# Kernel optimization log

Measured on AMD Instinct MI355X. Metric: run time of the kernel, lower is better.

## Reference

```python
import jax, jax.numpy as jnp
import numpy as np

B, IN, N, K = 8192, 1024, 4096, 409
BN_EPS = 1e-5
BOOST_STRENGTH = 1.0


def setup_inputs() -> dict:
    key = jax.random.key(0)
    k1, k2, k3, k4, k5 = jax.random.split(key, 5)
    x = jax.random.normal(k1, (B, IN), dtype=jnp.float32)
    W = jax.random.normal(k2, (N, IN), dtype=jnp.float32) * 0.03
    b = jax.random.normal(k3, (N,), dtype=jnp.float32) * 0.01
    wmask = jax.random.randint(k4, (N, IN), 0, 2, dtype=jnp.int32)
    dutyCycle = jax.random.uniform(k5, (N,), dtype=jnp.float32) * (K / N) * 2.0
    return {"x": x, "W": W, "b": b, "wmask": wmask, "dutyCycle": dutyCycle, "k": K}


def reference(x, W, b, wmask, dutyCycle, k):
    n = W.shape[0]
    # rezeroWeights: enforce fixed weight sparsity pattern
    Wm = W * wmask.astype(W.dtype)
    # Linear
    y = jnp.einsum("bi,ni->bn", x, Wm) + b
    # BatchNorm1d(affine=False), training mode: batch mean / biased variance
    mean = jnp.mean(y, axis=0)
    var = jnp.mean(jnp.square(y - mean), axis=0)
    y = (y - mean) / jnp.sqrt(var + BN_EPS)
    # KWinners with duty-cycle boosting (k < n path)
    targetDensity = jnp.float32(k) / n
    boostFactors = jnp.exp((targetDensity - dutyCycle) * BOOST_STRENGTH)
    boosted = jax.lax.stop_gradient(y) * boostFactors  # [B, n]
    _, idx = jax.lax.top_k(boosted, k)                 # [B, k]
    rows = jnp.arange(y.shape[0])[:, None]
    out = jnp.zeros_like(y).at[rows, idx].set(jnp.take_along_axis(y, idx, axis=1))
    return out
```

## Files before the change

### kernel.cpp

```cpp
#include <hip/hip_runtime.h>

#define BATCH 8192
#define INF   1024
#define NF    4096
#define BN_EPS 1e-5
#define NT    32

typedef __attribute__((ext_vector_type(8))) short short8v;
typedef __attribute__((ext_vector_type(4))) float f32x4;

#define FENCE asm volatile("" ::: "memory")
#define BARRIER do { FENCE; __builtin_amdgcn_s_barrier(); FENCE; } while (0)

__global__ void zero_ws(double* __restrict__ p) {
    p[blockIdx.x * 256 + threadIdx.x] = 0.0;
}

__device__ __forceinline__ void split3(float x, ushort& h0, ushort& h1, ushort& h2) {
    const unsigned u0 = __float_as_uint(x) & 0xFFFF0000u;
    const float    r1 = x - __uint_as_float(u0);
    const unsigned u1 = __float_as_uint(r1) & 0xFFFF0000u;
    const float    r2 = r1 - __uint_as_float(u1);
    h0 = (ushort)(u0 >> 16);
    h1 = (ushort)(u1 >> 16);
    h2 = (ushort)(__float_as_uint(r2) >> 16);
}

__global__ __launch_bounds__(256) void split_x_kernel(
    const float* __restrict__ X, ushort* __restrict__ xs)
{
    const size_t base = ((size_t)blockIdx.x * 256 + threadIdx.x) * 8;
    const size_t LS = (size_t)BATCH * INF;
    const float4 v0 = *(const float4*)(X + base);
    const float4 v1 = *(const float4*)(X + base + 4);
    const float v[8] = {v0.x, v0.y, v0.z, v0.w, v1.x, v1.y, v1.z, v1.w};
    short8v s0, s1, s2;
#pragma unroll
    for (int i = 0; i < 8; ++i) {
        ushort h0, h1, h2;
        split3(v[i], h0, h1, h2);
        s0[i] = (short)h0; s1[i] = (short)h1; s2[i] = (short)h2;
    }
    *(short8v*)&xs[base]          = s0;
    *(short8v*)&xs[base + LS]     = s1;
    *(short8v*)&xs[base + 2 * LS] = s2;
}

__global__ __launch_bounds__(256) void split_w_kernel(
    const float* __restrict__ W, const int* __restrict__ Mk, ushort* __restrict__ wsp)
{
    const size_t base = ((size_t)blockIdx.x * 256 + threadIdx.x) * 8;
    const size_t LS = (size_t)NF * INF;
    const float4 v0 = *(const float4*)(W + base);
    const float4 v1 = *(const float4*)(W + base + 4);
    const int4   m0 = *(const int4*)(Mk + base);
    const int4   m1 = *(const int4*)(Mk + base + 4);
    const float v[8] = {v0.x * (float)m0.x, v0.y * (float)m0.y,
                        v0.z * (float)m0.z, v0.w * (float)m0.w,
                        v1.x * (float)m1.x, v1.y * (float)m1.y,
                        v1.z * (float)m1.z, v1.w * (float)m1.w};
    short8v s0, s1, s2;
#pragma unroll
    for (int i = 0; i < 8; ++i) {
        ushort h0, h1, h2;
        split3(v[i], h0, h1, h2);
        s0[i] = (short)h0; s1[i] = (short)h1; s2[i] = (short)h2;
    }
    *(short8v*)&wsp[base]          = s0;
    *(short8v*)&wsp[base + LS]     = s1;
    *(short8v*)&wsp[base + 2 * LS] = s2;
}

__device__ __forceinline__ void gload16(const ushort* g, ushort* l) {
    __builtin_amdgcn_global_load_lds(
        (const __attribute__((address_space(1))) void*)g,
        (__attribute__((address_space(3))) void*)l, 16, 0, 0);
}

__global__ __launch_bounds__(512) void gemm_mfma_fuse(
    const ushort* __restrict__ Xs, const ushort* __restrict__ Wsp,
    const float* __restrict__ bias, float* __restrict__ Y,
    double* __restrict__ dsum, double* __restrict__ dsqs)
{
    extern __shared__ ushort sm[];
    const size_t LSX = (size_t)BATCH * INF;
    const size_t LSW = (size_t)NF * INF;

    const int t    = threadIdx.x;
    const int row0 = blockIdx.y * 128;
    const int col0 = blockIdx.x * 128;

    const int l   = t & 63;
    const int l15 = l & 15;
    const int hi  = l >> 4;
    const int wid = t >> 6;
    const int wm  = wid >> 1;
    const int wn  = wid & 1;

    const int srow  = t >> 2;
    const int sunit = (t & 3) ^ ((t >> 3) & 3);
    const int uoff = (hi ^ ((l15 >> 1) & 3)) << 3;

    f32x4  acc[2][4];
    double mst[2][4][4];
#pragma unroll
    for (int mf = 0; mf < 2; ++mf)
#pragma unroll
        for (int nf = 0; nf < 4; ++nf) {
            acc[mf][nf] = (f32x4){0.f, 0.f, 0.f, 0.f};
#pragma unroll
            for (int r = 0; r < 4; ++r) mst[mf][nf][r] = 0.0;
        }

#define PB(b, p) (sm + (b) * 24576 + (p) * 4096)

#pragma unroll
    for (int tt = 0; tt < 2; ++tt) {
#pragma unroll
        for (int p = 0; p < 3; ++p)
            gload16(Xs + (size_t)p * LSX + (size_t)(row0 + srow) * INF + tt * 32 + sunit * 8,
                    PB(tt, p) + (size_t)t * 8);
#pragma unroll
        for (int p = 0; p < 3; ++p)
            gload16(Wsp + (size_t)p * LSW + (size_t)(col0 + srow) * INF + tt * 32 + sunit * 8,
                    PB(tt, 3 + p) + (size_t)t * 8);
    }
    asm volatile("s_waitcnt vmcnt(6)" ::: "memory");
    BARRIER;

#define TILE(tt, CUR, DST) do {                                               \
    if ((tt) + 2 < NT) {                                                      \
        const int kof_ = ((tt) + 2) * 32;                                     \
        _Pragma("unroll")                                                     \
        for (int p = 0; p < 3; ++p)                                           \
            gload16(Xs + (size_t)p * LSX + (size_t)(row0 + srow) * INF + kof_ + sunit * 8, \
                    PB(DST, p) + (size_t)t * 8);                              \
        _Pragma("unroll")                                                     \
        for (int p = 0; p < 3; ++p)                                           \
            gload16(Wsp + (size_t)p * LSW + (size_t)(col0 + srow) * INF + kof_ + sunit * 8, \
                    PB(DST, 3 + p) + (size_t)t * 8);                          \
    }                                                                         \
    short8v A_[2][3], B_[4][3];                                               \
    _Pragma("unroll")                                                         \
    for (int mf = 0; mf < 2; ++mf) {                                          \
        const int ra = (wm * 32 + mf * 16 + l15) * 32 + uoff;                 \
        _Pragma("unroll")                                                     \
        for (int p = 0; p < 3; ++p)                                           \
            A_[mf][p] = *(const short8v*)&PB(CUR, p)[ra];                     \
    }                                                                         \
    _Pragma("unroll")                                                         \
    for (int nf = 0; nf < 4; ++nf) {                                          \
        const int rb = (wn * 64 + nf * 16 + l15) * 32 + uoff;                 \
        _Pragma("unroll")                                                     \
        for (int p = 0; p < 3; ++p)                                           \
            B_[nf][p] = *(const short8v*)&PB(CUR, 3 + p)[rb];                 \
    }                                                                         \
    __builtin_amdgcn_s_setprio(1);                                            \
    _Pragma("unroll")                                                         \
    for (int mf = 0; mf < 2; ++mf)                                            \
        _Pragma("unroll")                                                     \
        for (int nf = 0; nf < 4; ++nf) {                                      \
            f32x4 c = acc[mf][nf];                                            \
            c = __builtin_amdgcn_mfma_f32_16x16x32_bf16(A_[mf][0], B_[nf][0], c, 0, 0, 0); \
            c = __builtin_amdgcn_mfma_f32_16x16x32_bf16(A_[mf][0], B_[nf][1], c, 0, 0, 0); \
            c = __builtin_amdgcn_mfma_f32_16x16x32_bf16(A_[mf][1], B_[nf][0], c, 0, 0, 0); \
            c = __builtin_amdgcn_mfma_f32_16x16x32_bf16(A_[mf][0], B_[nf][2], c, 0, 0, 0); \
            c = __builtin_amdgcn_mfma_f32_16x16x32_bf16(A_[mf][1], B_[nf][1], c, 0, 0, 0); \
            c = __builtin_amdgcn_mfma_f32_16x16x32_bf16(A_[mf][2], B_[nf][0], c, 0, 0, 0); \
            acc[mf][nf] = c;                                                  \
        }                                                                     \
    __builtin_amdgcn_s_setprio(0);                                            \
    if ((tt) & 1) {                                                           \
        _Pragma("unroll")                                                     \
        for (int mf = 0; mf < 2; ++mf)                                        \
            _Pragma("unroll")                                                 \
            for (int nf = 0; nf < 4; ++nf) {                                  \
                _Pragma("unroll")                                             \
                for (int r = 0; r < 4; ++r)                                   \
                    mst[mf][nf][r] += (double)acc[mf][nf][r];                 \
                acc[mf][nf] = (f32x4){0.f, 0.f, 0.f, 0.f};                    \
            }                                                                 \
    }                                                                         \
    if ((tt) < NT - 2)       { asm volatile("s_waitcnt vmcnt(6)" ::: "memory"); } \
    else if ((tt) == NT - 2) { asm volatile("s_waitcnt vmcnt(0)" ::: "memory"); } \
    BARRIER;                                                                  \
} while (0)

    for (int tb = 0; tb + 3 <= NT; tb += 3) {
        TILE(tb,     0, 2);
        TILE(tb + 1, 1, 0);
        TILE(tb + 2, 2, 1);
    }
    TILE(30, 0, 2);
    TILE(31, 1, 0);
#undef TILE
#undef PB

    double* sdsum = (double*)sm;
    double* sdsqs = sdsum + 16 * 128;
    const int grp = wm * 4 + hi;
#pragma unroll
    for (int nf = 0; nf < 4; ++nf) {
        const int colL = wn * 64 + nf * 16 + l15;
        const int colc = col0 + colL;
        const double bb = (double)bias[colc];
        double s = 0.0, q = 0.0;
#pragma unroll
        for (int mf = 0; mf < 2; ++mf)
#pragma unroll
            for (int r = 0; r < 4; ++r) {
                const int roww = row0 + wm * 32 + mf * 16 + hi * 4 + r;
                const float yval = (float)(mst[mf][nf][r] + bb);
                Y[(size_t)roww * NF + colc] = yval;
                s += (double)yval;
                q += (double)yval * (double)yval;
            }
        sdsum[grp * 128 + colL] = s;
        sdsqs[grp * 128 + colL] = q;
    }
    __syncthreads();
    if (t < 128) {
        double s = 0.0;
#pragma unroll
        for (int g = 0; g < 16; ++g) s += sdsum[g * 128 + t];
        atomicAdd(&dsum[col0 + t], s);
    } else if (t < 256) {
        const int c = t - 128;
        double q = 0.0;
#pragma unroll
        for (int g = 0; g < 16; ++g) q += sdsqs[g * 128 + c];
        atomicAdd(&dsqs[col0 + c], q);
    }
}

__global__ __launch_bounds__(512) void gemm_mfma_split(
    const float* __restrict__ X, const float* __restrict__ W,
    const int* __restrict__ Mk, const float* __restrict__ bias,
    float* __restrict__ Y)
{
    __shared__ __align__(16) ushort a0s[128 * 40];
    __shared__ __align__(16) ushort a1s[128 * 40];
    __shared__ __align__(16) ushort a2s[128 * 40];
    __shared__ __align__(16) ushort b0s[128 * 40];
    __shared__ __align__(16) ushort b1s[128 * 40];
    __shared__ __align__(16) ushort b2s[128 * 40];

    const int t = threadIdx.x;
    const int row0 = blockIdx.y * 128;
    const int col0 = blockIdx.x * 128;
    const int srow = t >> 2;
    const int skb  = (t & 3) * 8;

    const float* Xp = X + (size_t)(row0 + srow) * INF + skb;
    const float* Wp = W + (size_t)(col0 + srow) * INF + skb;
    const int*   Mp = Mk + (size_t)(col0 + srow) * INF + skb;

    const int l   = t & 63;
    const int l15 = l & 15;
    const int hi  = l >> 4;
    const int wid = t >> 6;
    const int wm  = wid >> 1;
    const int wn  = wid & 1;

    f32x4  acc[2][4];
    double sh[2][4][4];
#pragma unroll
    for (int mf = 0; mf < 2; ++mf)
#pragma unroll
        for (int nf = 0; nf < 4; ++nf) {
            acc[mf][nf] = (f32x4){0.f, 0.f, 0.f, 0.f};
#pragma unroll
            for (int r = 0; r < 4; ++r) sh[mf][nf][r] = 0.0;
        }

    float4 xA0 = *(const float4*)(Xp);
    float4 xA1 = *(const float4*)(Xp + 4);
    float4 wB0 = *(const float4*)(Wp);
    float4 wB1 = *(const float4*)(Wp + 4);
    int4   mB0 = *(const int4*)(Mp);
    int4   mB1 = *(const int4*)(Mp + 4);

    for (int k0 = 0; k0 < INF; k0 += 32) {
        __syncthreads();
        {
            const float v[8] = {xA0.x, xA0.y, xA0.z, xA0.w, xA1.x, xA1.y, xA1.z, xA1.w};
            short8v s0, s1, s2;
#pragma unroll
            for (int i = 0; i < 8; ++i) {
                ushort h0, h1, h2;
                split3(v[i], h0, h1, h2);
                s0[i] = (short)h0; s1[i] = (short)h1; s2[i] = (short)h2;
            }
            const int off = srow * 40 + skb;
            *(short8v*)&a0s[off] = s0;
            *(short8v*)&a1s[off] = s1;
            *(short8v*)&a2s[off] = s2;
        }
        {
            const float wv[8] = {wB0.x * (float)mB0.x, wB0.y * (float)mB0.y,
                                 wB0.z * (float)mB0.z, wB0.w * (float)mB0.w,
                                 wB1.x * (float)mB1.x, wB1.y * (float)mB1.y,
                                 wB1.z * (float)mB1.z, wB1.w * (float)mB1.w};
            short8v s0, s1, s2;
#pragma unroll
            for (int i = 0; i < 8; ++i) {
                ushort h0, h1, h2;
                split3(wv[i], h0, h1, h2);
                s0[i] = (short)h0; s1[i] = (short)h1; s2[i] = (short)h2;
            }
            const int off = srow * 40 + skb;
            *(short8v*)&b0s[off] = s0;
            *(short8v*)&b1s[off] = s1;
            *(short8v*)&b2s[off] = s2;
        }
        __syncthreads();

        if (k0 + 32 < INF) {
            const int kn = k0 + 32;
            xA0 = *(const float4*)(Xp + kn);
            xA1 = *(const float4*)(Xp + kn + 4);
            wB0 = *(const float4*)(Wp + kn);
            wB1 = *(const float4*)(Wp + kn + 4);
            mB0 = *(const int4*)(Mp + kn);
            mB1 = *(const int4*)(Mp + kn + 4);
        }

        short8v A[2][3], B[4][3];
#pragma unroll
        for (int mf = 0; mf < 2; ++mf) {
            const int roff = (wm * 32 + mf * 16 + l15) * 40 + hi * 8;
            A[mf][0] = *(const short8v*)&a0s[roff];
            A[mf][1] = *(const short8v*)&a1s[roff];
            A[mf][2] = *(const short8v*)&a2s[roff];
        }
#pragma unroll
        for (int nf = 0; nf < 4; ++nf) {
            const int roff = (wn * 64 + nf * 16 + l15) * 40 + hi * 8;
            B[nf][0] = *(const short8v*)&b0s[roff];
            B[nf][1] = *(const short8v*)&b1s[roff];
            B[nf][2] = *(const short8v*)&b2s[roff];
        }

#pragma unroll
        for (int mf = 0; mf < 2; ++mf)
#pragma unroll
            for (int nf = 0; nf < 4; ++nf) {
                f32x4 c = acc[mf][nf];
                c = __builtin_amdgcn_mfma_f32_16x16x32_bf16(A[mf][0], B[nf][0], c, 0, 0, 0);
                c = __builtin_amdgcn_mfma_f32_16x16x32_bf16(A[mf][0], B[nf][1], c, 0, 0, 0);
                c = __builtin_amdgcn_mfma_f32_16x16x32_bf16(A[mf][1], B[nf][0], c, 0, 0, 0);
                c = __builtin_amdgcn_mfma_f32_16x16x32_bf16(A[mf][0], B[nf][2], c, 0, 0, 0);
                c = __builtin_amdgcn_mfma_f32_16x16x32_bf16(A[mf][1], B[nf][1], c, 0, 0, 0);
                c = __builtin_amdgcn_mfma_f32_16x16x32_bf16(A[mf][2], B[nf][0], c, 0, 0, 0);
                acc[mf][nf] = c;
            }

        if (k0 & 32) {
#pragma unroll
            for (int mf = 0; mf < 2; ++mf)
#pragma unroll
                for (int nf = 0; nf < 4; ++nf) {
#pragma unroll
                    for (int r = 0; r < 4; ++r) sh[mf][nf][r] += (double)acc[mf][nf][r];
                    acc[mf][nf] = (f32x4){0.f, 0.f, 0.f, 0.f};
                }
        }
    }

#pragma unroll
    for (int mf = 0; mf < 2; ++mf)
#pragma unroll
        for (int nf = 0; nf < 4; ++nf) {
            const int col = col0 + wn * 64 + nf * 16 + l15;
            const double bb = (double)bias[col];
#pragma unroll
            for (int r = 0; r < 4; ++r) {
                const int row = row0 + wm * 32 + mf * 16 + hi * 4 + r;
                Y[(size_t)row * NF + col] = (float)(sh[mf][nf][r] + bb);
            }
        }
}

__global__ __launch_bounds__(256) void stats_partial(
    const float* __restrict__ Y, double* __restrict__ dsum, double* __restrict__ dsqs)
{
    const int col = blockIdx.x * 256 + threadIdx.x;
    const int r0  = blockIdx.y * 256;
    double s = 0.0, ss = 0.0;
    for (int i = 0; i < 256; ++i) {
        const float v = Y[(size_t)(r0 + i) * NF + col];
        s  += (double)v;
        ss += (double)v * (double)v;
    }
    atomicAdd(&dsum[col], s);
    atomicAdd(&dsqs[col], ss);
}

__global__ __launch_bounds__(256) void stats_final(
    const double* __restrict__ dsum, const double* __restrict__ dsqs,
    const float* __restrict__ duty, const int* __restrict__ kp,
    double* __restrict__ mean64, double* __restrict__ rstd64, double* __restrict__ boost64,
    float* __restrict__ mean32, float* __restrict__ rstd32, float* __restrict__ boost32)
{
    const int c = blockIdx.x * 256 + threadIdx.x;
    const double m   = dsum[c] / (double)BATCH;
    const double var = dsqs[c] / (double)BATCH - m * m;
    const double rs  = 1.0 / sqrt(var + (double)BN_EPS);
    const double td  = (double)(*kp) / (double)NF;
    const double bf  = exp(td - (double)duty[c]);
    mean64[c] = m;  rstd64[c] = rs;  boost64[c] = bf;
    mean32[c] = (float)m; rstd32[c] = (float)rs; boost32[c] = (float)bf;
}

#define BAND 1e-4f
#define MAXCAND 64
#define LCAP 512

__global__ __launch_bounds__(256) void topk_kernel(
    const float* __restrict__ mean32, const float* __restrict__ rstd32,
    const float* __restrict__ boost32,
    const double* __restrict__ mean64, const double* __restrict__ rstd64,
    const double* __restrict__ boost64,
    const int* __restrict__ kp,
    const float* __restrict__ X, const float* __restrict__ W,
    const int* __restrict__ Mk, const float* __restrict__ bias,
    float* __restrict__ Y)
{
    __shared__ float    yv[NF];
    __shared__ unsigned keys[NF];
    __shared__ unsigned hist[256];
    __shared__ unsigned scan[256];
    __shared__ unsigned wtot[4];
    __shared__ unsigned s_bin, s_below;
    __shared__ int      s_cnt;
    __shared__ unsigned lkey[LCAP];
    __shared__ double   red[256];
    __shared__ int      s_ncand, s_H;
    __shared__ int      cand_idx[MAXCAND];
    __shared__ double   cand_val[MAXCAND];
    __shared__ unsigned char cand_pick[MAXCAND];

    const int r = blockIdx.x;
    const int t = threadIdx.x;
    const int K = *kp;
    const int lane = t & 63;
    const int w    = t >> 6;

    for (int j = 0; j < 4; ++j) {
        const int n = j * 1024 + t * 4;
        const float4 v  = *(const float4*)&Y[(size_t)r * NF + n];
        const float4 mm = *(const float4*)&mean32[n];
        const float4 rs = *(const float4*)&rstd32[n];
        const float4 bo = *(const float4*)&boost32[n];
        const float yb[4] = {(v.x - mm.x) * rs.x, (v.y - mm.y) * rs.y,
                             (v.z - mm.z) * rs.z, (v.w - mm.w) * rs.w};
        const float bsv[4] = {yb[0] * bo.x, yb[1] * bo.y, yb[2] * bo.z, yb[3] * bo.w};
#pragma unroll
        for (int q = 0; q < 4; ++q) {
            yv[n + q] = yb[q];
            unsigned u = __float_as_uint(bsv[q]);
            u ^= (u & 0x80000000u) ? 0xFFFFFFFFu : 0x80000000u;
            keys[n + q] = u;
        }
    }
    __syncthreads();

#define SUFFIX_SCAN() do {                                                    \
    unsigned v_ = hist[t];                                                    \
    _Pragma("unroll")                                                         \
    for (int off_ = 1; off_ < 64; off_ <<= 1) {                               \
        const unsigned o_ = __shfl_down(v_, off_, 64);                        \
        if (lane + off_ < 64) v_ += o_;                                       \
    }                                                                         \
    if (lane == 0) wtot[w] = v_;                                              \
    __syncthreads();                                                          \
    unsigned add_ = 0;                                                        \
    for (int ww_ = w + 1; ww_ < 4; ++ww_) add_ += wtot[ww_];                  \
    scan[t] = v_ + add_;                                                      \
    __syncthreads();                                                          \
} while (0)

    hist[t] = 0u;
    __syncthreads();
    for (int j = 0; j < 16; ++j)
        atomicAdd(&hist[keys[j * 256 + t] >> 24], 1u);
    __syncthreads();
    SUFFIX_SCAN();
    int remaining = K;
    if (scan[t] >= (unsigned)remaining &&
        (t == 255 || scan[t + 1] < (unsigned)remaining)) {
        s_bin = (unsigned)t;
        s_below = (t == 255) ? 0u : scan[t + 1];
    }
    if (t == 0) s_cnt = 0;
    __syncthreads();
    const unsigned b1 = s_bin;
    unsigned curval = b1 << 24;
    unsigned curmask = 0xFF000000u;
    remaining -= (int)s_below;
    __syncthreads();

    for (int j = 0; j < 16; ++j) {
        const unsigned u = keys[j * 256 + t];
        if ((u >> 24) == b1) {
            const int slot = atomicAdd(&s_cnt, 1);
            if (slot < LCAP) lkey[slot] = u;
        }
    }
    __syncthreads();
    const bool smallbin = (s_cnt <= LCAP);
    const int cnt = s_cnt;

    for (int pass = 2; pass >= 0; --pass) {
        const int sh = pass * 8;
        hist[t] = 0u;
        __syncthreads();
        if (smallbin) {
            for (int i = t; i < cnt; i += 256) {
                const unsigned u = lkey[i];
                if ((u & curmask) == curval)
                    atomicAdd(&hist[(u >> sh) & 255u], 1u);
            }
        } else {
            for (int j = 0; j < 16; ++j) {
                const unsigned u = keys[j * 256 + t];
                if ((u & curmask) == curval)
                    atomicAdd(&hist[(u >> sh) & 255u], 1u);
            }
        }
        __syncthreads();
        SUFFIX_SCAN();
        if (scan[t] >= (unsigned)remaining &&
            (t == 255 || scan[t + 1] < (unsigned)remaining)) {
            s_bin = (unsigned)t;
            s_below = (t == 255) ? 0u : scan[t + 1];
        }
        __syncthreads();
        curval |= (s_bin << sh);
        curmask |= (255u << sh);
        remaining -= (int)s_below;
        __syncthreads();
    }
#undef SUFFIX_SCAN

    const unsigned T = curval;
    const unsigned vT = (T & 0x80000000u) ? (T ^ 0x80000000u) : ~T;
    const float cut32 = __uint_as_float(vT);
    const float cutHi = cut32 + BAND;
    const float cutLo = cut32 - BAND;

    if (t == 0) { s_ncand = 0; s_H = 0; }
    __syncthreads();
    int locH = 0;
    for (int j = 0; j < 16; ++j) {
        const int n = j * 256 + t;
        const float b = yv[n] * boost32[n];
        if (b > cutHi) {
            locH++;
        } else if (b >= cutLo) {
            const int slot = atomicAdd(&s_ncand, 1);
            if (slot < MAXCAND) cand_idx[slot] = n;
        }
    }
    atomicAdd(&s_H, locH);
    __syncthreads();
    const int H = s_H;
    const bool overflow = (s_ncand > MAXCAND);
    const int ncand = overflow ? MAXCAND : s_ncand;
    int need = K - H;
    if (need < 0) need = 0;

    if (!overflow) {
        for (int c = 0; c < ncand; ++c) {
            const int n = cand_idx[c];
            const float* xr = X + (size_t)r * INF;
            const float* wn = W + (size_t)n * INF;
            const int*   mn = Mk + (size_t)n * INF;
            double s = 0.0;
            for (int i = t; i < INF; i += 256)
                s += (double)xr[i] * (double)(wn[i] * (float)mn[i]);
            red[t] = s;
            __syncthreads();
            for (int off = 128; off > 0; off >>= 1) {
                if (t < off) red[t] += red[t + off];
                __syncthreads();
            }
            if (t == 0) {
                const double y64 = red[0] + (double)bias[n];
                cand_val[c] = (y64 - mean64[n]) * rstd64[n] * boost64[n];
                cand_pick[c] = 0;
            }
            __syncthreads();
        }
        if (t == 0) {
            for (int p = 0; p < need; ++p) {
                int best = -1;
                for (int c = 0; c < ncand; ++c) {
                    if (cand_pick[c]) continue;
                    if (best < 0 || cand_val[c] > cand_val[best] ||
                        (cand_val[c] == cand_val[best] && cand_idx[c] < cand_idx[best]))
                        best = c;
                }
                if (best < 0) break;
                cand_pick[best] = 1;
            }
        }
        __syncthreads();
        for (int j = 0; j < 16; ++j) {
            const int n = j * 256 + t;
            const float b = yv[n] * boost32[n];
            keys[n] = (b > cutHi) ? 1u : 0u;
        }
        __syncthreads();
        if (t < ncand && cand_pick[t]) keys[cand_idx[t]] = 1u;
        __syncthreads();
    } else {
        const int fneed = remaining;
        unsigned cntk = 0u;
        for (int j = 0; j < 16; ++j) cntk += (keys[t * 16 + j] == T) ? 1u : 0u;
        scan[t] = cntk;
        __syncthreads();
        for (int off = 1; off < 256; off <<= 1) {
            const unsigned add = (t >= off) ? scan[t - off] : 0u;
            __syncthreads();
            scan[t] += add;
            __syncthreads();
        }
        unsigned rank = scan[t] - cntk;
        for (int j = 0; j < 16; ++j) {
            const int n = t * 16 + j;
            const unsigned u = keys[n];
            bool sel;
            if (u == T) { sel = ((int)rank < fneed); rank++; }
            else        { sel = (u > T); }
            keys[n] = sel ? 1u : 0u;
        }
        __syncthreads();
    }

    for (int j = 0; j < 4; ++j) {
        const int n = j * 1024 + t * 4;
        float4 o;
        o.x = keys[n + 0] ? yv[n + 0] : 0.0f;
        o.y = keys[n + 1] ? yv[n + 1] : 0.0f;
        o.z = keys[n + 2] ? yv[n + 2] : 0.0f;
        o.w = keys[n + 3] ? yv[n + 3] : 0.0f;
        *(float4*)&Y[(size_t)r * NF + n] = o;
    }
}

extern "C" void kernel_launch(void* const* d_in, const int* in_sizes, int n_in,
                              void* d_out, int out_size, void* d_ws, size_t ws_size,
                              hipStream_t stream)
{
    const float* x     = (const float*)d_in[0];
    const float* W     = (const float*)d_in[1];
    const float* b     = (const float*)d_in[2];
    const int*   wmask = (const int*)d_in[3];
    const float* duty  = (const float*)d_in[4];
    const int*   kp    = (const int*)d_in[5];
    float* out = (float*)d_out;

    const size_t SPLIT_X_ELTS = (size_t)3 * BATCH * INF;
    const size_t SPLIT_W_ELTS = (size_t)3 * NF * INF;
    const size_t STATS_BYTES  = (size_t)5 * NF * sizeof(double) + (size_t)3 * NF * sizeof(float);
    const size_t NEED_FAST    = (SPLIT_X_ELTS + SPLIT_W_ELTS) * sizeof(ushort) + STATS_BYTES;
    const bool fast = (ws_size >= NEED_FAST);

    ushort* xs  = (ushort*)d_ws;
    ushort* wsp = xs + SPLIT_X_ELTS;
    char* statbase = fast ? (char*)(wsp + SPLIT_W_ELTS) : (char*)d_ws;

    double* dsum    = (double*)statbase;
    double* dsqs    = dsum + NF;
    double* mean64  = dsqs + NF;
    double* rstd64  = mean64 + NF;
    double* boost64 = rstd64 + NF;
    float*  mean32  = (float*)(boost64 + NF);
    float*  rstd32  = mean32 + NF;
    float*  boost32 = rstd32 + NF;

    hipLaunchKernelGGL(zero_ws, dim3(2 * NF / 256), dim3(256), 0, stream, dsum);

    if (fast) {
        hipLaunchKernelGGL(split_x_kernel, dim3(BATCH * INF / 8 / 256), dim3(256), 0, stream,
                           x, xs);
        hipLaunchKernelGGL(split_w_kernel, dim3(NF * INF / 8 / 256), dim3(256), 0, stream,
                           W, wmask, wsp);
        hipFuncSetAttribute((const void*)gemm_mfma_fuse,
                            hipFuncAttributeMaxDynamicSharedMemorySize, 147456);
        hipLaunchKernelGGL(gemm_mfma_fuse, dim3(NF / 128, BATCH / 128), dim3(512), 147456,
                           stream, xs, wsp, b, out, dsum, dsqs);
    } else {
        hipLaunchKernelGGL(gemm_mfma_split, dim3(NF / 128, BATCH / 128), dim3(512), 0, stream,
                           x, W, wmask, b, out);
        hipLaunchKernelGGL(stats_partial, dim3(NF / 256, BATCH / 256), dim3(256), 0, stream,
                           out, dsum, dsqs);
    }

    hipLaunchKernelGGL(stats_final, dim3(NF / 256), dim3(256), 0, stream,
                       dsum, dsqs, duty, kp,
                       mean64, rstd64, boost64, mean32, rstd32, boost32);
    hipLaunchKernelGGL(topk_kernel, dim3(BATCH), dim3(256), 0, stream,
                       mean32, rstd32, boost32, mean64, rstd64, boost64, kp,
                       x, W, wmask, b, out);
}
```

Baseline: 558.3 us.

## Merge prep kernels and stats zeroing, streamline top-k key marking

Folds the stats-buffer zeroing and the separate x and W split kernels into one prep launch, so the fast path saves two kernel launches. In the top-k kernel, the selection flags are written during the candidate scan, which removes a later pass that recomputed the boosted values. The tie-breaking path now recomputes the order-preserving keys from yv and boost because the keys array has been overwritten. LCAP is raised to 768 so larger bins can use the compact candidate list, at the cost of more shared memory.

```diff
diff --git a/kernel.cpp b/kernel.cpp
--- a/kernel.cpp
+++ b/kernel.cpp
@@ -11,10 +11,6 @@
 
 #define FENCE asm volatile("" ::: "memory")
 #define BARRIER do { FENCE; __builtin_amdgcn_s_barrier(); FENCE; } while (0)
-
-__global__ void zero_ws(double* __restrict__ p) {
-    p[blockIdx.x * 256 + threadIdx.x] = 0.0;
-}
 
 __device__ __forceinline__ void split3(float x, ushort& h0, ushort& h1, ushort& h2) {
     const unsigned u0 = __float_as_uint(x) & 0xFFFF0000u;
@@ -26,49 +22,60 @@
     h2 = (ushort)(__float_as_uint(r2) >> 16);
 }
 
-__global__ __launch_bounds__(256) void split_x_kernel(
-    const float* __restrict__ X, ushort* __restrict__ xs)
+__global__ __launch_bounds__(256) void prep_kernel(
+    const float* __restrict__ X, const float* __restrict__ W,
+    const int* __restrict__ Mk,
+    ushort* __restrict__ xs, ushort* __restrict__ wsp,
+    double* __restrict__ dz)
 {
-    const size_t base = ((size_t)blockIdx.x * 256 + threadIdx.x) * 8;
-    const size_t LS = (size_t)BATCH * INF;
-    const float4 v0 = *(const float4*)(X + base);
-    const float4 v1 = *(const float4*)(X + base + 4);
-    const float v[8] = {v0.x, v0.y, v0.z, v0.w, v1.x, v1.y, v1.z, v1.w};
-    short8v s0, s1, s2;
-#pragma unroll
-    for (int i = 0; i < 8; ++i) {
-        ushort h0, h1, h2;
-        split3(v[i], h0, h1, h2);
-        s0[i] = (short)h0; s1[i] = (short)h1; s2[i] = (short)h2;
-    }
-    *(short8v*)&xs[base]          = s0;
-    *(short8v*)&xs[base + LS]     = s1;
-    *(short8v*)&xs[base + 2 * LS] = s2;
-}
-
-__global__ __launch_bounds__(256) void split_w_kernel(
-    const float* __restrict__ W, const int* __restrict__ Mk, ushort* __restrict__ wsp)
-{
-    const size_t base = ((size_t)blockIdx.x * 256 + threadIdx.x) * 8;
-    const size_t LS = (size_t)NF * INF;
-    const float4 v0 = *(const float4*)(W + base);
-    const float4 v1 = *(const float4*)(W + base + 4);
-    const int4   m0 = *(const int4*)(Mk + base);
-    const int4   m1 = *(const int4*)(Mk + base + 4);
-    const float v[8] = {v0.x * (float)m0.x, v0.y * (float)m0.y,
-                        v0.z * (float)m0.z, v0.w * (float)m0.w,
-                        v1.x * (float)m1.x, v1.y * (float)m1.y,
-                        v1.z * (float)m1.z, v1.w * (float)m1.w};
-    short8v s0, s1, s2;
-#pragma unroll
-    for (int i = 0; i < 8; ++i) {
-        ushort h0, h1, h2;
-        split3(v[i], h0, h1, h2);
-        s0[i] = (short)h0; s1[i] = (short)h1; s2[i] = (short)h2;
-    }
-    *(short8v*)&wsp[base]          = s0;
-    *(short8v*)&wsp[base + LS]     = s1;
-    *(short8v*)&wsp[base + 2 * LS] = s2;
+    const int blk = blockIdx.x;
+    const int t   = threadIdx.x;
+    if (blk == 0) {
+#pragma unroll
+        for (int i = 0; i < 32; ++i) dz[i * 256 + t] = 0.0;
+    }
+    if (blk < 4096) {
+        const size_t base = ((size_t)blk * 256 + t) * 8;
+        const size_t LS = (size_t)BATCH * INF;
+        const float4 v0 = *(const float4*)(X + base);
+        const float4 v1 = *(const float4*)(X + base + 4);
+        const float v[8] = {v0.x, v0.y, v0.z, v0.w, v1.x, v1.y, v1.z, v1.w};
+        short8v s0, s1, s2;
+#pragma unroll
+        for (int i = 0; i < 8; ++i) {
+            ushort h0, h1, h2;
+            split3(v[i], h0, h1, h2);
+            s0[i] = (short)h0; s1[i] = (short)h1; s2[i] = (short)h2;
+        }
+        *(short8v*)&xs[base]          = s0;
+        *(short8v*)&xs[base + LS]     = s1;
+        *(short8v*)&xs[base + 2 * LS] = s2;
+    } else {
+        const size_t base = ((size_t)(blk - 4096) * 256 + t) * 8;
+        const size_t LS = (size_t)NF * INF;
+        const float4 v0 = *(const float4*)(W + base);
+        const float4 v1 = *(const float4*)(W + base + 4);
+        const int4   m0 = *(const int4*)(Mk + base);
+        const int4   m1 = *(const int4*)(Mk + base + 4);
+        const float v[8] = {v0.x * (float)m0.x, v0.y * (float)m0.y,
+                            v0.z * (float)m0.z, v0.w * (float)m0.w,
+                            v1.x * (float)m1.x, v1.y * (float)m1.y,
+                            v1.z * (float)m1.z, v1.w * (float)m1.w};
+        short8v s0, s1, s2;
+#pragma unroll
+        for (int i = 0; i < 8; ++i) {
+            ushort h0, h1, h2;
+            split3(v[i], h0, h1, h2);
+            s0[i] = (short)h0; s1[i] = (short)h1; s2[i] = (short)h2;
+        }
+        *(short8v*)&wsp[base]          = s0;
+        *(short8v*)&wsp[base + LS]     = s1;
+        *(short8v*)&wsp[base + 2 * LS] = s2;
+    }
+}
+
+__global__ void zero_ws(double* __restrict__ p) {
+    p[blockIdx.x * 256 + threadIdx.x] = 0.0;
 }
 
 __device__ __forceinline__ void gload16(const ushort* g, ushort* l) {
@@ -414,7 +421,7 @@
 
 #define BAND 1e-4f
 #define MAXCAND 64
-#define LCAP 512
+#define LCAP 768
 
 __global__ __launch_bounds__(256) void topk_kernel(
     const float* __restrict__ mean32, const float* __restrict__ rstd32,
@@ -509,7 +516,7 @@
     }
     __syncthreads();
     const bool smallbin = (s_cnt <= LCAP);
-    const int cnt = s_cnt;
+    const int cnt = smallbin ? s_cnt : 0;
 
     for (int pass = 2; pass >= 0; --pass) {
         const int sh = pass * 8;
@@ -555,12 +562,15 @@
     for (int j = 0; j < 16; ++j) {
         const int n = j * 256 + t;
         const float b = yv[n] * boost32[n];
+        unsigned fl = 0u;
         if (b > cutHi) {
             locH++;
+            fl = 1u;
         } else if (b >= cutLo) {
             const int slot = atomicAdd(&s_ncand, 1);
             if (slot < MAXCAND) cand_idx[slot] = n;
         }
+        keys[n] = fl;
     }
     atomicAdd(&s_H, locH);
     __syncthreads();
@@ -606,18 +616,17 @@
             }
         }
         __syncthreads();
-        for (int j = 0; j < 16; ++j) {
-            const int n = j * 256 + t;
-            const float b = yv[n] * boost32[n];
-            keys[n] = (b > cutHi) ? 1u : 0u;
-        }
-        __syncthreads();
         if (t < ncand && cand_pick[t]) keys[cand_idx[t]] = 1u;
         __syncthreads();
     } else {
         const int fneed = remaining;
         unsigned cntk = 0u;
-        for (int j = 0; j < 16; ++j) cntk += (keys[t * 16 + j] == T) ? 1u : 0u;
+        for (int j = 0; j < 16; ++j) {
+            const int n = t * 16 + j;
+            unsigned u = __float_as_uint(yv[n] * boost32[n]);
+            u ^= (u & 0x80000000u) ? 0xFFFFFFFFu : 0x80000000u;
+            cntk += (u == T) ? 1u : 0u;
+        }
         scan[t] = cntk;
         __syncthreads();
         for (int off = 1; off < 256; off <<= 1) {
@@ -629,7 +638,8 @@
         unsigned rank = scan[t] - cntk;
         for (int j = 0; j < 16; ++j) {
             const int n = t * 16 + j;
-            const unsigned u = keys[n];
+            unsigned u = __float_as_uint(yv[n] * boost32[n]);
+            u ^= (u & 0x80000000u) ? 0xFFFFFFFFu : 0x80000000u;
             bool sel;
             if (u == T) { sel = ((int)rank < fneed); rank++; }
             else        { sel = (u > T); }
@@ -680,18 +690,15 @@
     float*  rstd32  = mean32 + NF;
     float*  boost32 = rstd32 + NF;
 
-    hipLaunchKernelGGL(zero_ws, dim3(2 * NF / 256), dim3(256), 0, stream, dsum);
-
     if (fast) {
-        hipLaunchKernelGGL(split_x_kernel, dim3(BATCH * INF / 8 / 256), dim3(256), 0, stream,
-                           x, xs);
-        hipLaunchKernelGGL(split_w_kernel, dim3(NF * INF / 8 / 256), dim3(256), 0, stream,
-                           W, wmask, wsp);
+        hipLaunchKernelGGL(prep_kernel, dim3(6144), dim3(256), 0, stream,
+                           x, W, wmask, xs, wsp, dsum);
         hipFuncSetAttribute((const void*)gemm_mfma_fuse,
                             hipFuncAttributeMaxDynamicSharedMemorySize, 147456);
         hipLaunchKernelGGL(gemm_mfma_fuse, dim3(NF / 128, BATCH / 128), dim3(512), 147456,
                            stream, xs, wsp, b, out, dsum, dsqs);
     } else {
+        hipLaunchKernelGGL(zero_ws, dim3(2 * NF / 256), dim3(256), 0, stream, dsum);
         hipLaunchKernelGGL(gemm_mfma_split, dim3(NF / 128, BATCH / 128), dim3(512), 0, stream,
                            x, W, wmask, b, out);
         hipLaunchKernelGGL(stats_partial, dim3(NF / 256, BATCH / 256), dim3(256), 0, stream,
```

Result: no change. 548.3 us (median of 2 runs) (-1.8%).
